# Kernel optimization log

Measured on AMD Instinct MI355X. Metric: run time of the kernel, lower is better.

The kernel has to match this reference:

```python
import jax, jax.numpy as jnp
import numpy as np

# Model dims: E experts, D model dim, H GLU hidden dim; B batch, S seq, K top-k experts/token
E, D, H = 8, 768, 2048
B, S, K = 2, 512, 2


def setup_inputs() -> dict:
    key = jax.random.key(0)
    k1, k2, k3, k4, k5 = jax.random.split(key, 5)
    scale_in = (1.0 / D) ** 0.5   # SwitchLinear init scale sqrt(1/input_dims)
    scale_h = (1.0 / H) ** 0.5
    x = jax.random.normal(k1, (B, S, D), dtype=jnp.float32)
    indices = jax.random.randint(k2, (B, S, K), 0, E)
    w_gate = jax.random.uniform(k3, (E, H, D), jnp.float32, -scale_in, scale_in)
    w_up = jax.random.uniform(k4, (E, H, D), jnp.float32, -scale_in, scale_in)
    w_down = jax.random.uniform(k5, (E, D, H), jnp.float32, -scale_h, scale_h)
    return {"x": x, "indices": indices, "w_gate": w_gate, "w_up": w_up, "w_down": w_down}


def reference(x, indices, w_gate, w_up, w_down):
    # x: (B,S,D), indices: (B,S,K) in [0,E). Output: (B,S,K,D) per-expert outputs.
    Bx, Sx, Dx = x.shape
    Kx = indices.shape[-1]
    nE = w_gate.shape[0]

    # dispatch: sort token-expert pairs by expert id (mirrors _gather_sort)
    flat_idx = indices.reshape(-1)              # (N,) with N = B*S*K
    order = jnp.argsort(flat_idx)
    idx_s = flat_idx[order]                     # sorted expert ids
    xt = x.reshape(-1, Dx)[order // Kx]         # (N, D) gathered token rows

    # grouped expert GLU: per token n, y = silu(x W_gate[e]^T) * (x W_up[e]^T) @ W_down[e]^T
    # implemented as a masked dense pass per expert (small fixed E loop),
    # which avoids materializing the (N,H,D) per-token weight gather of the original.
    out = jnp.zeros((xt.shape[0], Dx), dtype=x.dtype)
    for e in range(nE):
        m = (idx_s == e)[:, None]
        up = xt @ w_up[e].T                     # (N, H)
        gate = xt @ w_gate[e].T                 # (N, H)
        h = jax.nn.silu(gate) * up              # SwiGLU: silu(gate) * up
        out = out + jnp.where(m, h @ w_down[e].T, jnp.zeros((), x.dtype))
    # combine: undo the sort (mirrors _scatter_unsort)
    inv_order = jnp.argsort(order)
    return out[inv_order].reshape(Bx, Sx, Kx, Dx)
```

## Files before the change

kernel.cpp:

```cpp
#include <hip/hip_runtime.h>


typedef unsigned short u16;
typedef unsigned int   u32;
typedef u16    u16x8 __attribute__((ext_vector_type(8)));
typedef __bf16 bf16x8 __attribute__((ext_vector_type(8)));
typedef float  f32x4 __attribute__((ext_vector_type(4)));

#define NE   8
#define DDIM 768
#define HDIM 2048
#define NTOT 2048
#define NTOK 1024
#define MAXT2 24

__device__ __forceinline__ u16 f2bf(float f) {
  return (u16)((__builtin_bit_cast(u32, f) + 0x8000u) >> 16);
}
__device__ __forceinline__ bf16x8 cvt8(float4 a, float4 b) {
  bf16x8 r;
  r[0] = (__bf16)a.x; r[1] = (__bf16)a.y; r[2] = (__bf16)a.z; r[3] = (__bf16)a.w;
  r[4] = (__bf16)b.x; r[5] = (__bf16)b.y; r[6] = (__bf16)b.z; r[7] = (__bf16)b.w;
  return r;
}
__device__ __forceinline__ f32x4 mfma(bf16x8 a, bf16x8 b, f32x4 c) {
  return __builtin_amdgcn_mfma_f32_16x16x32_bf16(a, b, c, 0, 0, 0);
}
__device__ __forceinline__ void gl16(const void* g, void* l) {
  __builtin_amdgcn_global_load_lds(
      (const __attribute__((address_space(1))) void*)g,
      (__attribute__((address_space(3))) void*)l, 16, 0, 0);
}
#define SCHEDB() __builtin_amdgcn_sched_barrier(0)
#define BAR()    __builtin_amdgcn_s_barrier()
#define VMW(n)   asm volatile("s_waitcnt vmcnt(" #n ")" ::: "memory")

#define RD8(arr, o_, r_, kb_) cvt8(                                              \
    *(const float4*)&(arr)[(o_) + (r_) * 32 + ((((kb_)*2    ) ^ ((r_)&7)) << 2)], \
    *(const float4*)&(arr)[(o_) + (r_) * 32 + ((((kb_)*2 + 1) ^ ((r_)&7)) << 2)])
#define RDB(arr, o_, r_, kb_) __builtin_bit_cast(bf16x8,                         \
    *(const u16x8*)&(arr)[(o_) + (r_) * 32 + (((kb_) ^ (((r_)>>1)&3)) << 3)])

__global__ __launch_bounds__(256) void moe_cvtx(const float* __restrict__ x,
                                                u16* __restrict__ xb) {
  const int i = (blockIdx.x * 256 + threadIdx.x) * 8;
  const float4 f0 = *(const float4*)(x + i);
  const float4 f1 = *(const float4*)(x + i + 4);
  *(uint4*)(xb + i) = __builtin_bit_cast(uint4, cvt8(f0, f1));
}

__global__ void moe_dispatch(const int* __restrict__ idx,
                             int* __restrict__ meta, int* __restrict__ perm) {
  __shared__ int s_cnt[NE];
  __shared__ int s_off[NE + 1];
  __shared__ int s_cur[NE];
  const int tid = threadIdx.x;
  if (tid < NE) { s_cnt[tid] = 0; s_cur[tid] = 0; }
  __syncthreads();
  for (int n = tid; n < NTOT; n += 256) atomicAdd(&s_cnt[idx[n]], 1);
  __syncthreads();
  if (tid == 0) {
    int a = 0;
    for (int e = 0; e < NE; ++e) { s_off[e] = a; a += s_cnt[e]; }
    s_off[NE] = a;
  }
  __syncthreads();
  for (int n = tid; n < NTOT; n += 256) {
    const int e = idx[n];
    perm[s_off[e] + atomicAdd(&s_cur[e], 1)] = n;
  }
  if (tid == 0) {
    int t2 = 0;
    for (int e = 0; e < NE; ++e) {
      for (int r0 = s_off[e]; r0 < s_off[e + 1]; r0 += 128) {
        meta[48 + t2] = e; meta[80 + t2] = r0; ++t2;
      }
    }
    meta[14] = t2;
  }
  if (tid < NE + 1) meta[tid] = s_off[tid];
}

__global__ __launch_bounds__(512, 2) void moe_stage1(
    const u16* __restrict__ xb, const int* __restrict__ perm,
    const int* __restrict__ meta, const float* __restrict__ wg,
    const float* __restrict__ wu, u16* __restrict__ hbuf) {
  const int t = blockIdx.x >> 5;
  if (t >= meta[14]) return;
  const int nt = blockIdx.x & 31;
  const int e = meta[48 + t];
  const int r0 = meta[80 + t];
  const int rows = min(128, meta[e + 1] - r0);

  __shared__ __align__(16) u16   sX[3 * 128 * 32];
  __shared__ __align__(16) float sG[3 * 64 * 32];
  __shared__ __align__(16) float sU[3 * 64 * 32];

  const int tid = threadIdx.x;
  const int lane = tid & 63;
  const int wv = tid >> 6;
  const int wm = (wv >> 1) * 32;
  const int wn = (wv & 1) * 32;
  const int fr = lane & 15, kb = lane >> 4;

  const int xr = tid >> 2;
  const int tok = perm[r0 + min(xr, rows - 1)] >> 1;
  const u16* gpX = xb + (size_t)tok * DDIM + (((tid & 3) ^ ((xr >> 1) & 3)) << 3);
  const int lbX = wv * 512;
  const int wr = tid >> 3;
  const float* gpG =
      wg + ((size_t)e * HDIM + nt * 64 + wr) * DDIM + (((tid & 7) ^ (wr & 7)) << 2);
  const float* gpU =
      wu + ((size_t)e * HDIM + nt * 64 + wr) * DDIM + (((tid & 7) ^ (wr & 7)) << 2);
  const int lbW = wv * 256;

  f32x4 aG[2][2] = {};
  f32x4 aU[2][2] = {};

#define S1_STAGE(slot, kt) do {                                   \
    gl16(gpX + (kt) * 32, &sX[(slot) * 4096 + lbX]);              \
    gl16(gpG + (kt) * 32, &sG[(slot) * 2048 + lbW]);              \
    gl16(gpU + (kt) * 32, &sU[(slot) * 2048 + lbW]);              \
  } while (0)

#define S1_COMPUTE(slot) do {                                     \
    const int su_ = (slot) * 4096, sf_ = (slot) * 2048;           \
    bf16x8 a0 = RDB(sX, su_, wm + fr, kb);                        \
    bf16x8 a1 = RDB(sX, su_, wm + 16 + fr, kb);                   \
    bf16x8 g0 = RD8(sG, sf_, wn + fr, kb);                        \
    bf16x8 g1 = RD8(sG, sf_, wn + 16 + fr, kb);                   \
    bf16x8 u0 = RD8(sU, sf_, wn + fr, kb);                        \
    bf16x8 u1 = RD8(sU, sf_, wn + 16 + fr, kb);                   \
    aG[0][0] = mfma(a0, g0, aG[0][0]);                            \
    aG[1][0] = mfma(a1, g0, aG[1][0]);                            \
    aG[0][1] = mfma(a0, g1, aG[0][1]);                            \
    aG[1][1] = mfma(a1, g1, aG[1][1]);                            \
    aU[0][0] = mfma(a0, u0, aU[0][0]);                            \
    aU[1][0] = mfma(a1, u0, aU[1][0]);                            \
    aU[0][1] = mfma(a0, u1, aU[0][1]);                            \
    aU[1][1] = mfma(a1, u1, aU[1][1]);                            \
  } while (0)

  S1_STAGE(0, 0);
  S1_STAGE(1, 1);
  VMW(3);
  BAR();

#pragma unroll 1
  for (int l = 0; l < 24; ++l) {
    if (l + 2 < 24) S1_STAGE((l + 2) % 3, l + 2);
    SCHEDB();
    S1_COMPUTE(l % 3);
    SCHEDB();
    if (l + 2 < 24) { VMW(3); BAR(); }
    else if (l == 22) { VMW(0); BAR(); }
  }

  const int crow = kb * 4, ccol = fr;
#pragma unroll
  for (int mi = 0; mi < 2; ++mi) {
#pragma unroll
    for (int ri = 0; ri < 4; ++ri) {
      const int lm = wm + mi * 16 + crow + ri;
      if (lm < rows) {
        u16* hb = hbuf + (size_t)(r0 + lm) * HDIM + nt * 64 + wn;
#pragma unroll
        for (int nj = 0; nj < 2; ++nj) {
          const float gv = aG[mi][nj][ri];
          const float uv = aU[mi][nj][ri];
          const float h = gv / (1.0f + __expf(-gv)) * uv;
          hb[nj * 16 + ccol] = f2bf(h);
        }
      }
    }
  }
}

__global__ __launch_bounds__(256, 3) void moe_stage2(
    const u16* __restrict__ hbuf, const int* __restrict__ perm,
    const int* __restrict__ meta, const float* __restrict__ wd,
    float* __restrict__ out) {
  const int t = blockIdx.x / 24;
  if (t >= meta[14]) return;
  const int rem = blockIdx.x - t * 24;
  const int ks = rem / 12;
  const int nt = rem - ks * 12;
  const int e = meta[48 + t];
  const int r0 = meta[80 + t];
  const int rows = min(128, meta[e + 1] - r0);

  __shared__ __align__(16) u16   sA[3 * 128 * 32];
  __shared__ __align__(16) float sB[3 * 64 * 32];

  const int tid = threadIdx.x;
  const int lane = tid & 63;
  const int wv = tid >> 6;
  const int wm = (wv >> 1) * 64;
  const int wn = (wv & 1) * 32;

  const u16* gpA[2];
  int lbA[2];
#pragma unroll
  for (int j = 0; j < 2; ++j) {
    const int r = wv * 32 + j * 16 + (lane >> 2);
    gpA[j] = hbuf + (size_t)(r0 + min(r, rows - 1)) * HDIM + ks * 1024 +
             (((lane & 3) ^ ((r >> 1) & 3)) << 3);
    lbA[j] = (wv * 32 + j * 16) * 32;
  }
  const float* gpB[2];
  int lbB[2];
#pragma unroll
  for (int j = 0; j < 2; ++j) {
    const int r = wv * 16 + j * 8 + (lane >> 3);
    gpB[j] = wd + ((size_t)e * DDIM + nt * 64 + r) * HDIM + ks * 1024 +
             (((lane & 7) ^ (r & 7)) << 2);
    lbB[j] = (wv * 16 + j * 8) * 32;
  }

  f32x4 acc[4][2] = {};

#define S2_STAGE(slot, kp) do {                                   \
    const int su_ = (slot) * 4096, sf_ = (slot) * 2048;           \
    const int ko_ = (kp) * 32;                                    \
    gl16(gpA[0] + ko_, &sA[su_ + lbA[0]]);                        \
    gl16(gpA[1] + ko_, &sA[su_ + lbA[1]]);                        \
    gl16(gpB[0] + ko_, &sB[sf_ + lbB[0]]);                        \
    gl16(gpB[1] + ko_, &sB[sf_ + lbB[1]]);                        \
  } while (0)

#define S2_COMPUTE(slot) do {                                     \
    const int su_ = (slot) * 4096, sf_ = (slot) * 2048;           \
    const int fr_ = lane & 15, kb_ = lane >> 4;                   \
    bf16x8 a0 = RDB(sA, su_, wm + fr_, kb_);                      \
    bf16x8 a1 = RDB(sA, su_, wm + 16 + fr_, kb_);                 \
    bf16x8 a2 = RDB(sA, su_, wm + 32 + fr_, kb_);                 \
    bf16x8 a3 = RDB(sA, su_, wm + 48 + fr_, kb_);                 \
    bf16x8 b0 = RD8(sB, sf_, wn + fr_, kb_);                      \
    bf16x8 b1 = RD8(sB, sf_, wn + 16 + fr_, kb_);                 \
    acc[0][0] = mfma(a0, b0, acc[0][0]);                          \
    acc[1][0] = mfma(a1, b0, acc[1][0]);                          \
    acc[2][0] = mfma(a2, b0, acc[2][0]);                          \
    acc[3][0] = mfma(a3, b0, acc[3][0]);                          \
    acc[0][1] = mfma(a0, b1, acc[0][1]);                          \
    acc[1][1] = mfma(a1, b1, acc[1][1]);                          \
    acc[2][1] = mfma(a2, b1, acc[2][1]);                          \
    acc[3][1] = mfma(a3, b1, acc[3][1]);                          \
  } while (0)

  S2_STAGE(0, 0);
  S2_STAGE(1, 1);
  VMW(4);
  BAR();

#pragma unroll 1
  for (int l = 0; l < 32; ++l) {
    if (l + 2 < 32) S2_STAGE((l + 2) % 3, l + 2);
    SCHEDB();
    S2_COMPUTE(l % 3);
    SCHEDB();
    if (l + 2 < 32) { VMW(4); BAR(); }
    else if (l == 30) { VMW(0); BAR(); }
  }

  const int crow = (lane >> 4) << 2;
  const int ccol = lane & 15;
#pragma unroll
  for (int mi = 0; mi < 4; ++mi) {
#pragma unroll
    for (int ri = 0; ri < 4; ++ri) {
      const int lm = wm + mi * 16 + crow + ri;
      if (lm < rows) {
        const int tok = perm[r0 + lm];
        float* orow = out + (size_t)tok * DDIM + nt * 64 + wn;
#pragma unroll
        for (int nj = 0; nj < 2; ++nj) {
          atomicAdd(&orow[nj * 16 + ccol], acc[mi][nj][ri]);
        }
      }
    }
  }
}

extern "C" void kernel_launch(void* const* d_in, const int* in_sizes, int n_in,
                              void* d_out, int out_size, void* d_ws, size_t ws_size,
                              hipStream_t stream) {
  const float* x  = (const float*)d_in[0];
  const int* idx  = (const int*)d_in[1];
  const float* wg = (const float*)d_in[2];
  const float* wu = (const float*)d_in[3];
  const float* wd = (const float*)d_in[4];
  float* out = (float*)d_out;

  int* iws = (int*)d_ws;
  int* meta = iws;
  int* perm = iws + 128;
  u16* xbuf = (u16*)((char*)d_ws + 16384);
  u16* hbuf = (u16*)((char*)d_ws + 16384 + (1 << 21));

  hipMemsetAsync(d_out, 0, (size_t)out_size * sizeof(float), stream);
  moe_cvtx<<<NTOK * DDIM / 2048, 256, 0, stream>>>(x, xbuf);
  moe_dispatch<<<1, 256, 0, stream>>>(idx, meta, perm);
  moe_stage1<<<MAXT2 * 32, 512, 0, stream>>>(xbuf, perm, meta, wg, wu, hbuf);
  moe_stage2<<<MAXT2 * 24, 256, 0, stream>>>(hbuf, perm, meta, wd, out);
}
```

Baseline: 98.35 us.

## Retile stage1 GEMM to 128x32 tiles with 256-thread blocks

Stage 1 changes from 512-thread blocks computing 128x64 output tiles to 256-thread blocks computing 128x32 tiles, doubling the grid. Each wave now covers 64 rows by 16 columns with four MFMA row fragments sharing one gate/up fragment. The goal is more blocks and better occupancy (3 blocks per CU, smaller weight LDS). The cost is that each block reloads the activation tile for half as many output columns, so X traffic to LDS doubles relative to the weight traffic.

```diff
diff --git a/kernel.cpp b/kernel.cpp
--- a/kernel.cpp
+++ b/kernel.cpp
@@ -81,69 +81,76 @@
   if (tid < NE + 1) meta[tid] = s_off[tid];
 }
 
-__global__ __launch_bounds__(512, 2) void moe_stage1(
+__global__ __launch_bounds__(256, 3) void moe_stage1(
     const u16* __restrict__ xb, const int* __restrict__ perm,
     const int* __restrict__ meta, const float* __restrict__ wg,
     const float* __restrict__ wu, u16* __restrict__ hbuf) {
-  const int t = blockIdx.x >> 5;
+  const int t = blockIdx.x >> 6;
   if (t >= meta[14]) return;
-  const int nt = blockIdx.x & 31;
+  const int nt = blockIdx.x & 63;
   const int e = meta[48 + t];
   const int r0 = meta[80 + t];
   const int rows = min(128, meta[e + 1] - r0);
 
   __shared__ __align__(16) u16   sX[3 * 128 * 32];
-  __shared__ __align__(16) float sG[3 * 64 * 32];
-  __shared__ __align__(16) float sU[3 * 64 * 32];
+  __shared__ __align__(16) float sG[3 * 32 * 32];
+  __shared__ __align__(16) float sU[3 * 32 * 32];
 
   const int tid = threadIdx.x;
   const int lane = tid & 63;
   const int wv = tid >> 6;
-  const int wm = (wv >> 1) * 32;
-  const int wn = (wv & 1) * 32;
+  const int wm = (wv >> 1) * 64;
+  const int wn = (wv & 1) * 16;
   const int fr = lane & 15, kb = lane >> 4;
 
-  const int xr = tid >> 2;
-  const int tok = perm[r0 + min(xr, rows - 1)] >> 1;
-  const u16* gpX = xb + (size_t)tok * DDIM + (((tid & 3) ^ ((xr >> 1) & 3)) << 3);
-  const int lbX = wv * 512;
+  const u16* gpX[2];
+  int lbX[2];
+#pragma unroll
+  for (int j = 0; j < 2; ++j) {
+    const int r = wv * 32 + j * 16 + (lane >> 2);
+    const int tok = perm[r0 + min(r, rows - 1)] >> 1;
+    gpX[j] = xb + (size_t)tok * DDIM + (((lane & 3) ^ ((r >> 1) & 3)) << 3);
+    lbX[j] = (wv * 32 + j * 16) * 32;
+  }
   const int wr = tid >> 3;
   const float* gpG =
-      wg + ((size_t)e * HDIM + nt * 64 + wr) * DDIM + (((tid & 7) ^ (wr & 7)) << 2);
+      wg + ((size_t)e * HDIM + nt * 32 + wr) * DDIM + (((tid & 7) ^ (wr & 7)) << 2);
   const float* gpU =
-      wu + ((size_t)e * HDIM + nt * 64 + wr) * DDIM + (((tid & 7) ^ (wr & 7)) << 2);
+      wu + ((size_t)e * HDIM + nt * 32 + wr) * DDIM + (((tid & 7) ^ (wr & 7)) << 2);
   const int lbW = wv * 256;
 
-  f32x4 aG[2][2] = {};
-  f32x4 aU[2][2] = {};
+  f32x4 aG[4] = {};
+  f32x4 aU[4] = {};
 
 #define S1_STAGE(slot, kt) do {                                   \
-    gl16(gpX + (kt) * 32, &sX[(slot) * 4096 + lbX]);              \
-    gl16(gpG + (kt) * 32, &sG[(slot) * 2048 + lbW]);              \
-    gl16(gpU + (kt) * 32, &sU[(slot) * 2048 + lbW]);              \
+    const int ko_ = (kt) * 32;                                    \
+    gl16(gpX[0] + ko_, &sX[(slot) * 4096 + lbX[0]]);              \
+    gl16(gpX[1] + ko_, &sX[(slot) * 4096 + lbX[1]]);              \
+    gl16(gpG + ko_, &sG[(slot) * 1024 + lbW]);                    \
+    gl16(gpU + ko_, &sU[(slot) * 1024 + lbW]);                    \
   } while (0)
 
 #define S1_COMPUTE(slot) do {                                     \
-    const int su_ = (slot) * 4096, sf_ = (slot) * 2048;           \
+    const int su_ = (slot) * 4096, sf_ = (slot) * 1024;           \
     bf16x8 a0 = RDB(sX, su_, wm + fr, kb);                        \
     bf16x8 a1 = RDB(sX, su_, wm + 16 + fr, kb);                   \
+    bf16x8 a2 = RDB(sX, su_, wm + 32 + fr, kb);                   \
+    bf16x8 a3 = RDB(sX, su_, wm + 48 + fr, kb);                   \
     bf16x8 g0 = RD8(sG, sf_, wn + fr, kb);                        \
-    bf16x8 g1 = RD8(sG, sf_, wn + 16 + fr, kb);                   \
     bf16x8 u0 = RD8(sU, sf_, wn + fr, kb);                        \
-    bf16x8 u1 = RD8(sU, sf_, wn + 16 + fr, kb);                   \
-    aG[0][0] = mfma(a0, g0, aG[0][0]);                            \
-    aG[1][0] = mfma(a1, g0, aG[1][0]);                            \
-    aG[0][1] = mfma(a0, g1, aG[0][1]);                            \
-    aG[1][1] = mfma(a1, g1, aG[1][1]);                            \
-    aU[0][0] = mfma(a0, u0, aU[0][0]);                            \
-    aU[1][0] = mfma(a1, u0, aU[1][0]);                            \
-    aU[0][1] = mfma(a0, u1, aU[0][1]);                            \
-    aU[1][1] = mfma(a1, u1, aU[1][1]);                            \
+    aG[0] = mfma(a0, g0, aG[0]);                                  \
+    aG[1] = mfma(a1, g0, aG[1]);                                  \
+    aG[2] = mfma(a2, g0, aG[2]);                                  \
+    aG[3] = mfma(a3, g0, aG[3]);                                  \
+    aU[0] = mfma(a0, u0, aU[0]);                                  \
+    aU[1] = mfma(a1, u0, aU[1]);                                  \
+    aU[2] = mfma(a2, u0, aU[2]);                                  \
+    aU[3] = mfma(a3, u0, aU[3]);                                  \
   } while (0)
 
   S1_STAGE(0, 0);
   S1_STAGE(1, 1);
-  VMW(3);
+  VMW(4);
   BAR();
 
 #pragma unroll 1
@@ -152,25 +159,22 @@
     SCHEDB();
     S1_COMPUTE(l % 3);
     SCHEDB();
-    if (l + 2 < 24) { VMW(3); BAR(); }
+    if (l + 2 < 24) { VMW(4); BAR(); }
     else if (l == 22) { VMW(0); BAR(); }
   }
 
   const int crow = kb * 4, ccol = fr;
 #pragma unroll
-  for (int mi = 0; mi < 2; ++mi) {
+  for (int mi = 0; mi < 4; ++mi) {
 #pragma unroll
     for (int ri = 0; ri < 4; ++ri) {
       const int lm = wm + mi * 16 + crow + ri;
       if (lm < rows) {
-        u16* hb = hbuf + (size_t)(r0 + lm) * HDIM + nt * 64 + wn;
-#pragma unroll
-        for (int nj = 0; nj < 2; ++nj) {
-          const float gv = aG[mi][nj][ri];
-          const float uv = aU[mi][nj][ri];
-          const float h = gv / (1.0f + __expf(-gv)) * uv;
-          hb[nj * 16 + ccol] = f2bf(h);
-        }
+        u16* hb = hbuf + (size_t)(r0 + lm) * HDIM + nt * 32 + wn;
+        const float gv = aG[mi][ri];
+        const float uv = aU[mi][ri];
+        const float h = gv / (1.0f + __expf(-gv)) * uv;
+        hb[ccol] = f2bf(h);
       }
     }
   }
@@ -300,6 +304,6 @@
   hipMemsetAsync(d_out, 0, (size_t)out_size * sizeof(float), stream);
   moe_cvtx<<<NTOK * DDIM / 2048, 256, 0, stream>>>(x, xbuf);
   moe_dispatch<<<1, 256, 0, stream>>>(idx, meta, perm);
-  moe_stage1<<<MAXT2 * 32, 512, 0, stream>>>(xbuf, perm, meta, wg, wu, hbuf);
+  moe_stage1<<<MAXT2 * 64, 256, 0, stream>>>(xbuf, perm, meta, wg, wu, hbuf);
   moe_stage2<<<MAXT2 * 24, 256, 0, stream>>>(hbuf, perm, meta, wd, out);
 }
```

Measured after the change: 94.67 us. 1.04x faster.
